# Kernel optimization log

Hardware: AMD Instinct MI355X
Metric: run time of the kernel (lower is better)

## Reference

```python
import jax, jax.numpy as jnp
import numpy as np
import math

H = 16          # n_head
N_EMBD = 1024
EPS = 1e-5      # torch LayerNorm default


def setup_inputs() -> dict:
    key = jax.random.key(0)
    ks = jax.random.split(key, 6)
    B, T, C = 2, 2048, 1024
    x = jax.random.normal(ks[0], (B, T, C), dtype=jnp.float32)
    s = 0.02  # GPT-2 style init scale keeps softmax logits sane
    Wq = jax.random.normal(ks[1], (C, N_EMBD), dtype=jnp.float32) * s
    Wk = jax.random.normal(ks[2], (C, N_EMBD), dtype=jnp.float32) * s
    Wv = jax.random.normal(ks[3], (C, N_EMBD), dtype=jnp.float32) * s
    Wo = jax.random.normal(ks[4], (N_EMBD, C), dtype=jnp.float32) * s
    return {
        "x": x,
        "Wq": Wq, "bq": jnp.zeros((N_EMBD,), jnp.float32),
        "Wk": Wk, "bk": jnp.zeros((N_EMBD,), jnp.float32),
        "Wv": Wv, "bv": jnp.zeros((N_EMBD,), jnp.float32),
        "Wo": Wo, "bo": jnp.zeros((C,), jnp.float32),
        "gamma": jnp.ones((C,), jnp.float32),
        "beta": jnp.zeros((C,), jnp.float32),
    }


def reference(x, Wq, bq, Wk, bk, Wv, bv, Wo, bo, gamma, beta):
    B, T, _ = x.shape
    Dh = N_EMBD // H
    # projections -> (B, H, T, Dh)
    def split_heads(y):
        return y.reshape(B, T, H, Dh).transpose(0, 2, 1, 3)
    q = split_heads(x @ Wq + bq)
    k = split_heads(x @ Wk + bk)
    v = split_heads(x @ Wv + bv)
    # naive causal attention: explicit (B,H,T,T) scores
    att = jnp.einsum("bhtd,bhsd->bhts", q, k) * (1.0 / math.sqrt(Dh))
    causal = jnp.tril(jnp.ones((T, T), dtype=bool))
    att = jnp.where(causal[None, None], att, -jnp.inf)
    att = jax.nn.softmax(att, axis=-1)
    o = jnp.einsum("bhts,bhsd->bhtd", att, v)
    o = o.transpose(0, 2, 1, 3).reshape(B, T, N_EMBD)
    y = o @ Wo + bo
    # LayerNorm (dropout is identity at p=0 / eval)
    mu = jnp.mean(y, axis=-1, keepdims=True)
    var = jnp.var(y, axis=-1, keepdims=True)
    return (y - mu) * jax.lax.rsqrt(var + EPS) * gamma + beta
```

## Files before the change

### kernel.cpp

```cpp
#include <hip/hip_runtime.h>
#include <stdint.h>
#include <stddef.h>

typedef __attribute__((ext_vector_type(8))) short short8;
typedef __attribute__((ext_vector_type(4))) float f32x4;
typedef __attribute__((ext_vector_type(16))) float f32x16;
typedef __attribute__((ext_vector_type(4))) unsigned short us4;
typedef __attribute__((ext_vector_type(4))) unsigned u32x4;

#define DEVI static __device__ __forceinline__

DEVI unsigned short f2bf(float f) {
  unsigned u = __builtin_bit_cast(unsigned, f);
  u += 0x7FFFu + ((u >> 16) & 1u);
  return (unsigned short)(u >> 16);
}

DEVI float bf2f(unsigned short u) {
  return __builtin_bit_cast(float, ((unsigned)u) << 16);
}

DEVI f32x4 mfma16(short8 a, short8 b, f32x4 c) {
  return __builtin_amdgcn_mfma_f32_16x16x32_bf16(a, b, c, 0, 0, 0);
}

DEVI f32x16 mfma32(short8 a, short8 b, f32x16 c) {
  return __builtin_amdgcn_mfma_f32_32x32x16_bf16(a, b, c, 0, 0, 0);
}

DEVI unsigned cvtpk(float lo, float hi) {
  unsigned r;
  asm("v_cvt_pk_bf16_f32 %0, %1, %2" : "=v"(r) : "v"(lo), "v"(hi));
  return r;
}

DEVI void plswap(unsigned& a, unsigned& b) {
  asm("v_permlane32_swap_b32 %0, %1" : "+v"(a), "+v"(b));
}

DEVI float ex2(float x) {
  float r;
  asm("v_exp_f32 %0, %1" : "=v"(r) : "v"(x));
  return r;
}

DEVI float mx3(float a, float b, float c) {
  float r;
  asm("v_max3_f32 %0, %1, %2, %3" : "=v"(r) : "v"(a), "v"(b), "v"(c));
  return r;
}

DEVI f32x16 zero16() {
  f32x16 z;
#pragma unroll
  for (int i = 0; i < 16; ++i) z[i] = 0.f;
  return z;
}

DEVI void glds16(const void* g, void* l) {
  __builtin_amdgcn_global_load_lds(
      (const __attribute__((address_space(1))) void*)g,
      (__attribute__((address_space(3))) void*)l, 16, 0, 0);
}

__global__ __launch_bounds__(256) void k_cvt_x(const float* __restrict__ x,
                                               unsigned short* __restrict__ xb) {
  size_t i = ((size_t)blockIdx.x * 256 + threadIdx.x) * 8;
  f32x4 a = *(const f32x4*)(x + i);
  f32x4 b = *(const f32x4*)(x + i + 4);
  short8 v;
#pragma unroll
  for (int j = 0; j < 4; ++j) {
    v[j] = (short)f2bf(a[j]);
    v[4 + j] = (short)f2bf(b[j]);
  }
  *(short8*)(xb + i) = v;
}

__global__ __launch_bounds__(256) void k_twT4(const float* __restrict__ W0,
                                              const float* __restrict__ W1,
                                              const float* __restrict__ W2,
                                              const float* __restrict__ W3,
                                              unsigned short* __restrict__ WT) {
  __shared__ float tile[64][65];
  const int z = blockIdx.z;
  const float* W = (z == 0) ? W0 : (z == 1) ? W1 : (z == 2) ? W2 : W3;
  unsigned short* out = WT + (size_t)z * 1024 * 1024;
  const int n0 = blockIdx.x * 64, k0 = blockIdx.y * 64;
  const int t = threadIdx.x, rr = t >> 4, cc = (t & 15) * 4;
#pragma unroll
  for (int i = 0; i < 4; ++i) {
    int row = i * 16 + rr;
    f32x4 v = *(const f32x4*)(W + (size_t)(k0 + row) * 1024 + n0 + cc);
#pragma unroll
    for (int j = 0; j < 4; ++j) tile[row][cc + j] = v[j];
  }
  __syncthreads();
#pragma unroll
  for (int i = 0; i < 4; ++i) {
    int nrow = i * 16 + rr;
    us4 u;
#pragma unroll
    for (int j = 0; j < 4; ++j) u[j] = f2bf(tile[cc + j][nrow]);
    *(us4*)(out + (size_t)(n0 + nrow) * 1024 + k0 + cc) = u;
  }
}

template <bool SWAP>
DEVI void gemm_core2(const unsigned short* __restrict__ A,
                     const unsigned short* __restrict__ Bt,
                     int mt, int nt, char* lds, f32x4 (&acc)[4][4]) {
  const int t = threadIdx.x;
  const int l = t & 63, c = l & 15, g = l >> 4;
  const int w = t >> 6, wr = w >> 1, wc = w & 1;
  const int srow = t >> 3;
  const int sxor = (((t & 7) ^ (srow & 7))) * 8;
  const unsigned short* Ab = A + (size_t)(mt * 128 + srow) * 1024 + sxor;
  const unsigned short* Bb = Bt + (size_t)(nt * 128 + srow) * 1024 + sxor;
  const int key = (c & 7);

  auto STAGE = [&](int kt, int buf) {
    char* lb = lds + buf * 32768;
#pragma unroll
    for (int i = 0; i < 4; ++i) {
      glds16(Ab + (size_t)i * 32 * 1024 + kt * 64, lb + i * 4096 + t * 16);
      glds16(Bb + (size_t)i * 32 * 1024 + kt * 64, lb + 16384 + i * 4096 + t * 16);
    }
  };

  STAGE(0, 0);
  asm volatile("s_waitcnt vmcnt(0)" ::: "memory");
  __builtin_amdgcn_s_barrier();
  asm volatile("" ::: "memory");
  for (int kt = 0; kt < 16; ++kt) {
    const int cur = kt & 1;
    if (kt < 15) STAGE(kt + 1, cur ^ 1);
    const char* lb = lds + cur * 32768;
#pragma unroll
    for (int ks = 0; ks < 2; ++ks) {
      short8 af[4], bfr[4];
#pragma unroll
      for (int m = 0; m < 4; ++m)
        af[m] = *(const short8*)(lb + (wr * 64 + m * 16 + c) * 128 +
                                 ((ks * 4 + g) ^ key) * 16);
#pragma unroll
      for (int n = 0; n < 4; ++n)
        bfr[n] = *(const short8*)(lb + 16384 + (wc * 64 + n * 16 + c) * 128 +
                                  ((ks * 4 + g) ^ key) * 16);
#pragma unroll
      for (int m = 0; m < 4; ++m)
#pragma unroll
        for (int n = 0; n < 4; ++n)
          acc[m][n] = SWAP ? mfma16(bfr[n], af[m], acc[m][n])
                           : mfma16(af[m], bfr[n], acc[m][n]);
    }
    asm volatile("s_waitcnt vmcnt(0)" ::: "memory");
    __builtin_amdgcn_s_barrier();
    asm volatile("" ::: "memory");
  }
}

__global__ __launch_bounds__(256) void k_gemm_qkv(
    const unsigned short* __restrict__ A,
    const unsigned short* __restrict__ Wf,
    const float* __restrict__ b0, const float* __restrict__ b1, const float* __restrict__ b2,
    unsigned short* __restrict__ O0, unsigned short* __restrict__ O1,
    unsigned short* __restrict__ O2) {
  __shared__ char lds[65536];
  const int mt = blockIdx.x, ntz = blockIdx.y;
  const int z = ntz >> 3, ntl = ntz & 7;
  const float* bias = (z == 0) ? b0 : (z == 1) ? b1 : b2;
  unsigned short* out = (z == 0) ? O0 : (z == 1) ? O1 : O2;
  f32x4 acc[4][4];
#pragma unroll
  for (int m = 0; m < 4; ++m)
#pragma unroll
    for (int n = 0; n < 4; ++n) acc[m][n] = (f32x4){0.f, 0.f, 0.f, 0.f};
  const int t = threadIdx.x, l = t & 63, c = l & 15, g = l >> 4;
  const int w = t >> 6, wr = w >> 1, wc = w & 1;
  if (z < 2) {
    gemm_core2<true>(A, Wf, mt, ntz, lds, acc);
    const float sc = (z == 0) ? 0.18033688011f : 1.0f;
#pragma unroll
    for (int n = 0; n < 4; ++n) {
      int colb = ntl * 128 + wc * 64 + n * 16 + 4 * g;
      f32x4 bv4 = *(const f32x4*)(bias + colb);
      int h = colb >> 6, d = colb & 63;
#pragma unroll
      for (int m = 0; m < 4; ++m) {
        int rowg = mt * 128 + wr * 64 + m * 16 + c;
        int b = rowg >> 11, tt = rowg & 2047;
        us4 u;
#pragma unroll
        for (int r = 0; r < 4; ++r) u[r] = f2bf((acc[m][n][r] + bv4[r]) * sc);
        *(us4*)(out + ((size_t)(b * 16 + h) * 2048 + tt) * 64 + d) = u;
      }
    }
  } else {
    gemm_core2<false>(A, Wf, mt, ntz, lds, acc);
#pragma unroll
    for (int n = 0; n < 4; ++n) {
      int colg = ntl * 128 + wc * 64 + n * 16 + c;
      float bvv = bias[colg];
      int h = colg >> 6, d = colg & 63;
#pragma unroll
      for (int m = 0; m < 4; ++m) {
        int rowg = mt * 128 + wr * 64 + m * 16 + 4 * g;
        int b = rowg >> 11, tt = rowg & 2047;
        us4 u;
#pragma unroll
        for (int r = 0; r < 4; ++r) u[r] = f2bf(acc[m][n][r] + bvv);
        *(us4*)(out + ((size_t)(b * 16 + h) * 64 + d) * 2048 + tt) = u;
      }
    }
  }
}

__global__ __launch_bounds__(256) void k_gemm_proj(const unsigned short* __restrict__ A,
                                                   const unsigned short* __restrict__ Bt,
                                                   const float* __restrict__ bias,
                                                   float* __restrict__ Y) {
  __shared__ char lds[65536];
  f32x4 acc[4][4];
#pragma unroll
  for (int m = 0; m < 4; ++m)
#pragma unroll
    for (int n = 0; n < 4; ++n) acc[m][n] = (f32x4){0.f, 0.f, 0.f, 0.f};
  const int mt = blockIdx.x, nt = blockIdx.y;
  gemm_core2<true>(A, Bt, mt, nt, lds, acc);
  const int t = threadIdx.x, l = t & 63, c = l & 15, g = l >> 4;
  const int w = t >> 6, wr = w >> 1, wc = w & 1;
#pragma unroll
  for (int n = 0; n < 4; ++n) {
    int colb = nt * 128 + wc * 64 + n * 16 + 4 * g;
    f32x4 bv4 = *(const f32x4*)(bias + colb);
#pragma unroll
    for (int m = 0; m < 4; ++m) {
      int rowg = mt * 128 + wr * 64 + m * 16 + c;
      f32x4 o;
#pragma unroll
      for (int r = 0; r < 4; ++r) o[r] = acc[m][n][r] + bv4[r];
      *(f32x4*)(Y + (size_t)rowg * 1024 + colb) = o;
    }
  }
}

__global__ __launch_bounds__(128) void k_attn5(const unsigned short* __restrict__ Q,
                                               const unsigned short* __restrict__ K,
                                               const unsigned short* __restrict__ VT,
                                               unsigned short* __restrict__ O,
                                               unsigned short* __restrict__ P,
                                               float* __restrict__ ML) {
  __shared__ char lds[32768];
  const int bid = blockIdx.x;
  int qt, c0, nt, mode, bh;
  if (bid < 512) {
    mode = 1; qt = 16 + (bid >> 5); c0 = 0; nt = 16; bh = bid & 31;
  } else {
    int rem = bid - 512;
    int v = 16 - (rem >> 6);
    int sub = rem & 63;
    bh = sub & 31;
    if (sub < 32) { mode = 0; qt = v - 1;  c0 = 0;  nt = v; }
    else          { mode = 2; qt = v + 15; c0 = 16; nt = v; }
  }
  const int t = threadIdx.x;
  const int w = t >> 6, l = t & 63;
  const int lq = l & 31, hi = l >> 5;
  const int q0 = qt * 64 + w * 32;
  const size_t kbase = (size_t)bh * 2048 * 64;
  const size_t vbase = (size_t)bh * 64 * 2048;
  const int srow = t >> 3;
  const int sx = ((t & 7) ^ (srow & 7)) * 8;

  short8 qf[4];
#pragma unroll
  for (int ds = 0; ds < 4; ++ds)
    qf[ds] = *(const short8*)(Q + kbase + (size_t)(q0 + lq) * 64 + 16 * ds + 8 * hi);

  auto STAGE = [&](int ktg, int buf) {
    const unsigned short* Kt = K + kbase + (size_t)ktg * 4096;
    const unsigned short* Vt = VT + vbase + ktg * 64;
    char* lb = lds + buf * 16384;
#pragma unroll
    for (int i = 0; i < 4; ++i) {
      int row = i * 16 + srow;
      glds16(Kt + (size_t)row * 64 + sx, lb + i * 2048 + t * 16);
      glds16(Vt + (size_t)row * 2048 + sx, lb + 8192 + i * 2048 + t * 16);
    }
  };

  f32x16 oacc[2];
  oacc[0] = zero16();
  oacc[1] = zero16();
  float m_s = -1e30f, l_s = 0.f;
  const int rx = lq & 7;

  STAGE(c0, 0);
  for (int kt = 0; kt < nt; ++kt) {
    asm volatile("s_waitcnt vmcnt(0)" ::: "memory");
    __builtin_amdgcn_s_barrier();
    asm volatile("" ::: "memory");
    if (kt + 1 < nt) STAGE(c0 + kt + 1, (kt + 1) & 1);
    const char* lb = lds + (kt & 1) * 16384;
    const int kv0 = (c0 + kt) * 64;
    short8 kf0[4], kf1[4];
#pragma unroll
    for (int ds = 0; ds < 4; ++ds) {
      int blk = ((ds * 2 + hi) ^ rx) * 16;
      kf0[ds] = *(const short8*)(lb + lq * 128 + blk);
      kf1[ds] = *(const short8*)(lb + (lq + 32) * 128 + blk);
    }
    f32x16 st0 = zero16(), st1 = zero16();
    __builtin_amdgcn_s_setprio(1);
#pragma unroll
    for (int ds = 0; ds < 4; ++ds) {
      st0 = mfma32(kf0[ds], qf[ds], st0);
      st1 = mfma32(kf1[ds], qf[ds], st1);
    }
    __builtin_amdgcn_s_setprio(0);
    short8 vf[2][4];
#pragma unroll
    for (int fd = 0; fd < 2; ++fd) {
      int d = fd * 32 + lq;
#pragma unroll
      for (int s = 0; s < 4; ++s)
        vf[fd][s] = *(const short8*)(lb + 8192 + d * 128 + (((s * 2 + hi) ^ rx) * 16));
    }
    if (mode != 1 && kt == nt - 1) {
      const int qg = q0 + lq;
#pragma unroll
      for (int r = 0; r < 16; ++r) {
        int kr = kv0 + (r & 3) + 8 * (r >> 2) + 4 * hi;
        if (kr > qg) st0[r] = -1e30f;
        if (kr + 32 > qg) st1[r] = -1e30f;
      }
    }
    float a8[8];
#pragma unroll
    for (int r = 0; r < 8; ++r)
      a8[r] = fmaxf(mx3(st0[r], st0[r + 8], st1[r]), st1[r + 8]);
    float mxv = mx3(mx3(a8[0], a8[1], a8[2]), mx3(a8[3], a8[4], a8[5]),
                    fmaxf(a8[6], a8[7]));
    mxv = fmaxf(mxv, __shfl_xor(mxv, 32, 64));
    if (!__all(mxv - m_s <= 11.5413f)) {
      float mnew = fmaxf(m_s, mxv);
      float corr = ex2(m_s - mnew);
      m_s = mnew;
      l_s *= corr;
#pragma unroll
      for (int r = 0; r < 16; ++r) {
        oacc[0][r] *= corr;
        oacc[1][r] *= corr;
      }
    }
    unsigned Wp[2][4][2];
    float gs[8];
#pragma unroll
    for (int f = 0; f < 2; ++f)
#pragma unroll
      for (int m4 = 0; m4 < 4; ++m4) {
        float p0 = ex2((f ? st1 : st0)[4 * m4 + 0] - m_s);
        float p1 = ex2((f ? st1 : st0)[4 * m4 + 1] - m_s);
        float p2 = ex2((f ? st1 : st0)[4 * m4 + 2] - m_s);
        float p3 = ex2((f ? st1 : st0)[4 * m4 + 3] - m_s);
        gs[f * 4 + m4] = (p0 + p1) + (p2 + p3);
        Wp[f][m4][0] = cvtpk(p0, p1);
        Wp[f][m4][1] = cvtpk(p2, p3);
      }
    float ps = ((gs[0] + gs[1]) + (gs[2] + gs[3])) + ((gs[4] + gs[5]) + (gs[6] + gs[7]));
    ps += __shfl_xor(ps, 32, 64);
    l_s += ps;
    __builtin_amdgcn_s_setprio(1);
#pragma unroll
    for (int s = 0; s < 4; ++s) {
      const int f = s >> 1, s2 = s & 1;
      unsigned a0 = Wp[f][2 * s2][0], b0 = Wp[f][2 * s2 + 1][0];
      unsigned a1 = Wp[f][2 * s2][1], b1 = Wp[f][2 * s2 + 1][1];
      plswap(a0, b0);
      plswap(a1, b1);
      u32x4 pw = {a0, a1, b0, b1};
      short8 pf = __builtin_bit_cast(short8, pw);
      oacc[0] = mfma32(vf[0][s], pf, oacc[0]);
      oacc[1] = mfma32(vf[1][s], pf, oacc[1]);
    }
    __builtin_amdgcn_s_setprio(0);
  }
  if (mode == 0) {
    const float inv = 1.0f / l_s;
    const int b = bh >> 4, h = bh & 15;
    unsigned short* orow = O + ((size_t)b * 2048 + q0 + lq) * 1024 + h * 64 + 4 * hi;
#pragma unroll
    for (int f = 0; f < 2; ++f)
#pragma unroll
      for (int m4 = 0; m4 < 4; ++m4) {
        us4 u;
#pragma unroll
        for (int rr = 0; rr < 4; ++rr) u[rr] = f2bf(oacc[f][4 * m4 + rr] * inv);
        *(us4*)(orow + f * 32 + m4 * 8) = u;
      }
  } else {
    const int pid = ((qt - 16) * 32 + bh) * 2 + (mode - 1);
    unsigned short* prow = P + (size_t)pid * 4096 + (w * 32 + lq) * 64 + 4 * hi;
#pragma unroll
    for (int f = 0; f < 2; ++f)
#pragma unroll
      for (int m4 = 0; m4 < 4; ++m4) {
        us4 u;
#pragma unroll
        for (int rr = 0; rr < 4; ++rr) u[rr] = f2bf(oacc[f][4 * m4 + rr]);
        *(us4*)(prow + f * 32 + m4 * 8) = u;
      }
    if (hi == 0) {
      ML[pid * 128 + w * 32 + lq] = m_s;
      ML[pid * 128 + 64 + w * 32 + lq] = l_s;
    }
  }
}

__global__ __launch_bounds__(64) void k_merge(const unsigned short* __restrict__ P,
                                              const float* __restrict__ ML,
                                              unsigned short* __restrict__ O) {
  const int blk = blockIdx.x;
  const int qt = 16 + (blk >> 5), bh = blk & 31;
  const int pidA = ((qt - 16) * 32 + bh) * 2, pidB = pidA + 1;
  const int r = threadIdx.x;
  float mA = ML[pidA * 128 + r], lA = ML[pidA * 128 + 64 + r];
  float mB = ML[pidB * 128 + r], lB = ML[pidB * 128 + 64 + r];
  float mM = fmaxf(mA, mB);
  float wA = ex2(mA - mM), wB = ex2(mB - mM);
  float inv = 1.f / (lA * wA + lB * wB);
  wA *= inv;
  wB *= inv;
  const unsigned short* pa = P + (size_t)pidA * 4096 + r * 64;
  const unsigned short* pb = P + (size_t)pidB * 4096 + r * 64;
  const int b = bh >> 4, h = bh & 15, q = qt * 64 + r;
  unsigned short* orow = O + ((size_t)b * 2048 + q) * 1024 + h * 64;
#pragma unroll
  for (int j = 0; j < 8; ++j) {
    short8 a = *(const short8*)(pa + j * 8);
    short8 c = *(const short8*)(pb + j * 8);
    short8 o;
#pragma unroll
    for (int k = 0; k < 8; ++k)
      o[k] = (short)f2bf(bf2f((unsigned short)a[k]) * wA +
                         bf2f((unsigned short)c[k]) * wB);
    *(short8*)(orow + j * 8) = o;
  }
}

__global__ __launch_bounds__(256) void k_ln(const float* __restrict__ Y,
                                            const float* __restrict__ gamma,
                                            const float* __restrict__ beta,
                                            float* __restrict__ out) {
  __shared__ float red[8];
  const int row = blockIdx.x, t = threadIdx.x, w = t >> 6, l = t & 63;
  const float* yr = Y + (size_t)row * 1024;
  f32x4 v = *(const f32x4*)(yr + t * 4);
  float s = v[0] + v[1] + v[2] + v[3];
  float ss = v[0] * v[0] + v[1] * v[1] + v[2] * v[2] + v[3] * v[3];
#pragma unroll
  for (int d = 1; d < 64; d <<= 1) {
    s += __shfl_xor(s, d, 64);
    ss += __shfl_xor(ss, d, 64);
  }
  if (l == 0) {
    red[w] = s;
    red[4 + w] = ss;
  }
  __syncthreads();
  s = red[0] + red[1] + red[2] + red[3];
  ss = red[4] + red[5] + red[6] + red[7];
  float mean = s * (1.f / 1024.f);
  float var = ss * (1.f / 1024.f) - mean * mean;
  float rstd = rsqrtf(var + 1e-5f);
  f32x4 gv = *(const f32x4*)(gamma + t * 4);
  f32x4 bv = *(const f32x4*)(beta + t * 4);
  f32x4 ov;
#pragma unroll
  for (int j = 0; j < 4; ++j) ov[j] = (v[j] - mean) * rstd * gv[j] + bv[j];
  *(f32x4*)(out + (size_t)row * 1024 + t * 4) = ov;
}

extern "C" void kernel_launch(void* const* d_in, const int* in_sizes, int n_in,
                              void* d_out, int out_size, void* d_ws, size_t ws_size,
                              hipStream_t stream) {
  (void)in_sizes; (void)n_in; (void)out_size; (void)ws_size;
  const float* x = (const float*)d_in[0];
  const float* Wq = (const float*)d_in[1];
  const float* bq = (const float*)d_in[2];
  const float* Wk = (const float*)d_in[3];
  const float* bk = (const float*)d_in[4];
  const float* Wv = (const float*)d_in[5];
  const float* bv = (const float*)d_in[6];
  const float* Wo = (const float*)d_in[7];
  const float* bo = (const float*)d_in[8];
  const float* gamma = (const float*)d_in[9];
  const float* beta = (const float*)d_in[10];
  char* ws = (char*)d_ws;
  const size_t MB = 1024 * 1024;
  unsigned short* xb = (unsigned short*)(ws);
  unsigned short* WT = (unsigned short*)(ws + 8 * MB);
  unsigned short* WoT = (unsigned short*)(ws + 14 * MB);
  unsigned short* Qb = (unsigned short*)(ws + 16 * MB);
  unsigned short* Kb = (unsigned short*)(ws + 24 * MB);
  unsigned short* VTb = (unsigned short*)(ws + 32 * MB);
  unsigned short* Ob = (unsigned short*)(ws + 40 * MB);
  float* Y = (float*)(ws + 16 * MB);
  unsigned short* Pp = (unsigned short*)(ws);
  float* MLp = (float*)(ws + 8 * MB);

  k_cvt_x<<<2048, 256, 0, stream>>>(x, xb);
  k_twT4<<<dim3(16, 16, 4), 256, 0, stream>>>(Wq, Wk, Wv, Wo, WT);
  k_gemm_qkv<<<dim3(32, 24), 256, 0, stream>>>(xb, WT, bq, bk, bv, Qb, Kb, VTb);
  k_attn5<<<1536, 128, 0, stream>>>(Qb, Kb, VTb, Ob, Pp, MLp);
  k_merge<<<512, 64, 0, stream>>>(Pp, MLp, Ob);
  k_gemm_proj<<<dim3(32, 8), 256, 0, stream>>>(Ob, WoT, bo, Y);
  k_ln<<<4096, 256, 0, stream>>>(Y, gamma, beta, (float*)d_out);
}
```

Measured before the change: 118.6 us.

## Halve attention KV tile to 32 and skip fully masked tiles per wave

The attention kernel now steps through keys in 32-row tiles instead of 64, so its LDS footprint halves and the V tile uses a new swizzled layout. Each wave gets its own trip count, letting the lower-query wave skip the last fully masked tile on diagonal blocks instead of computing and discarding it. The cost is twice as many loop iterations, each with a barrier and a smaller MFMA batch. The smaller LDS use may allow more blocks to be resident per CU.

```diff
diff --git a/kernel.cpp b/kernel.cpp
--- a/kernel.cpp
+++ b/kernel.cpp
@@ -245,24 +245,24 @@
   }
 }
 
-__global__ __launch_bounds__(128) void k_attn5(const unsigned short* __restrict__ Q,
+__global__ __launch_bounds__(128) void k_attn6(const unsigned short* __restrict__ Q,
                                                const unsigned short* __restrict__ K,
                                                const unsigned short* __restrict__ VT,
                                                unsigned short* __restrict__ O,
                                                unsigned short* __restrict__ P,
                                                float* __restrict__ ML) {
-  __shared__ char lds[32768];
+  __shared__ char lds[16384];
   const int bid = blockIdx.x;
-  int qt, c0, nt, mode, bh;
+  int qt, c0, NT, mode, bh;
   if (bid < 512) {
-    mode = 1; qt = 16 + (bid >> 5); c0 = 0; nt = 16; bh = bid & 31;
+    mode = 1; qt = 16 + (bid >> 5); c0 = 0; NT = 32; bh = bid & 31;
   } else {
     int rem = bid - 512;
     int v = 16 - (rem >> 6);
     int sub = rem & 63;
     bh = sub & 31;
-    if (sub < 32) { mode = 0; qt = v - 1;  c0 = 0;  nt = v; }
-    else          { mode = 2; qt = v + 15; c0 = 16; nt = v; }
+    if (sub < 32) { mode = 0; qt = v - 1;  c0 = 0;  NT = 2 * v; }
+    else          { mode = 2; qt = v + 15; c0 = 32; NT = 2 * v; }
   }
   const int t = threadIdx.x;
   const int w = t >> 6, l = t & 63;
@@ -270,8 +270,8 @@
   const int q0 = qt * 64 + w * 32;
   const size_t kbase = (size_t)bh * 2048 * 64;
   const size_t vbase = (size_t)bh * 64 * 2048;
-  const int srow = t >> 3;
-  const int sx = ((t & 7) ^ (srow & 7)) * 8;
+  const int srow = t >> 3, sblk = t & 7;
+  const int my_nt = (mode == 1) ? 32 : (NT - 1 + w);
 
   short8 qf[4];
 #pragma unroll
@@ -279,14 +279,17 @@
     qf[ds] = *(const short8*)(Q + kbase + (size_t)(q0 + lq) * 64 + 16 * ds + 8 * hi);
 
   auto STAGE = [&](int ktg, int buf) {
-    const unsigned short* Kt = K + kbase + (size_t)ktg * 4096;
-    const unsigned short* Vt = VT + vbase + ktg * 64;
-    char* lb = lds + buf * 16384;
-#pragma unroll
-    for (int i = 0; i < 4; ++i) {
+    const unsigned short* Kt = K + kbase + (size_t)ktg * 32 * 64;
+    char* lb = lds + buf * 8192;
+#pragma unroll
+    for (int i = 0; i < 2; ++i) {
       int row = i * 16 + srow;
-      glds16(Kt + (size_t)row * 64 + sx, lb + i * 2048 + t * 16);
-      glds16(Vt + (size_t)row * 2048 + sx, lb + 8192 + i * 2048 + t * 16);
+      glds16(Kt + (size_t)row * 64 + (size_t)((sblk ^ (row & 7)) * 8),
+             lb + i * 2048 + t * 16);
+      int bp = sblk ^ (row & 7);
+      int d = row * 2 + (bp >> 2);
+      glds16(VT + vbase + (size_t)d * 2048 + (size_t)(ktg * 32 + (bp & 3) * 8),
+             lb + 4096 + i * 2048 + t * 16);
     }
   };
 
@@ -297,94 +300,86 @@
   const int rx = lq & 7;
 
   STAGE(c0, 0);
-  for (int kt = 0; kt < nt; ++kt) {
+  for (int kt = 0; kt < NT; ++kt) {
     asm volatile("s_waitcnt vmcnt(0)" ::: "memory");
     __builtin_amdgcn_s_barrier();
     asm volatile("" ::: "memory");
-    if (kt + 1 < nt) STAGE(c0 + kt + 1, (kt + 1) & 1);
-    const char* lb = lds + (kt & 1) * 16384;
-    const int kv0 = (c0 + kt) * 64;
-    short8 kf0[4], kf1[4];
-#pragma unroll
-    for (int ds = 0; ds < 4; ++ds) {
-      int blk = ((ds * 2 + hi) ^ rx) * 16;
-      kf0[ds] = *(const short8*)(lb + lq * 128 + blk);
-      kf1[ds] = *(const short8*)(lb + (lq + 32) * 128 + blk);
-    }
-    f32x16 st0 = zero16(), st1 = zero16();
-    __builtin_amdgcn_s_setprio(1);
-#pragma unroll
-    for (int ds = 0; ds < 4; ++ds) {
-      st0 = mfma32(kf0[ds], qf[ds], st0);
-      st1 = mfma32(kf1[ds], qf[ds], st1);
-    }
-    __builtin_amdgcn_s_setprio(0);
-    short8 vf[2][4];
-#pragma unroll
-    for (int fd = 0; fd < 2; ++fd) {
-      int d = fd * 32 + lq;
-#pragma unroll
-      for (int s = 0; s < 4; ++s)
-        vf[fd][s] = *(const short8*)(lb + 8192 + d * 128 + (((s * 2 + hi) ^ rx) * 16));
-    }
-    if (mode != 1 && kt == nt - 1) {
-      const int qg = q0 + lq;
-#pragma unroll
-      for (int r = 0; r < 16; ++r) {
-        int kr = kv0 + (r & 3) + 8 * (r >> 2) + 4 * hi;
-        if (kr > qg) st0[r] = -1e30f;
-        if (kr + 32 > qg) st1[r] = -1e30f;
-      }
-    }
-    float a8[8];
-#pragma unroll
-    for (int r = 0; r < 8; ++r)
-      a8[r] = fmaxf(mx3(st0[r], st0[r + 8], st1[r]), st1[r + 8]);
-    float mxv = mx3(mx3(a8[0], a8[1], a8[2]), mx3(a8[3], a8[4], a8[5]),
-                    fmaxf(a8[6], a8[7]));
-    mxv = fmaxf(mxv, __shfl_xor(mxv, 32, 64));
-    if (!__all(mxv - m_s <= 11.5413f)) {
-      float mnew = fmaxf(m_s, mxv);
-      float corr = ex2(m_s - mnew);
-      m_s = mnew;
-      l_s *= corr;
-#pragma unroll
-      for (int r = 0; r < 16; ++r) {
-        oacc[0][r] *= corr;
-        oacc[1][r] *= corr;
-      }
-    }
-    unsigned Wp[2][4][2];
-    float gs[8];
-#pragma unroll
-    for (int f = 0; f < 2; ++f)
+    if (kt + 1 < NT) STAGE(c0 + kt + 1, (kt + 1) & 1);
+    if (kt < my_nt) {
+      const char* lb = lds + (kt & 1) * 8192;
+      const int kv0 = (c0 + kt) * 32;
+      short8 kf[4];
+#pragma unroll
+      for (int ds = 0; ds < 4; ++ds)
+        kf[ds] = *(const short8*)(lb + lq * 128 + (((ds * 2 + hi) ^ rx) * 16));
+      f32x16 st = zero16();
+      __builtin_amdgcn_s_setprio(1);
+#pragma unroll
+      for (int ds = 0; ds < 4; ++ds) st = mfma32(kf[ds], qf[ds], st);
+      __builtin_amdgcn_s_setprio(0);
+      short8 vf[2][2];
+#pragma unroll
+      for (int fd = 0; fd < 2; ++fd) {
+        int d2 = fd * 16 + (lq >> 1);
+        int vkey = d2 & 7;
+#pragma unroll
+        for (int s = 0; s < 2; ++s)
+          vf[fd][s] = *(const short8*)(lb + 4096 + d2 * 128 +
+                                       ((((lq & 1) * 4 + s * 2 + hi) ^ vkey) * 16));
+      }
+      if (mode != 1 && kt == my_nt - 1) {
+        const int qg = q0 + lq;
+#pragma unroll
+        for (int r = 0; r < 16; ++r) {
+          int kr = kv0 + (r & 3) + 8 * (r >> 2) + 4 * hi;
+          if (kr > qg) st[r] = -1e30f;
+        }
+      }
+      float a0 = mx3(st[0], st[1], st[2]), a1 = mx3(st[3], st[4], st[5]);
+      float a2 = mx3(st[6], st[7], st[8]), a3 = mx3(st[9], st[10], st[11]);
+      float a4 = mx3(st[12], st[13], st[14]);
+      float mxv = fmaxf(mx3(a0, a1, a2), mx3(a3, a4, st[15]));
+      mxv = fmaxf(mxv, __shfl_xor(mxv, 32, 64));
+      if (!__all(mxv - m_s <= 11.5413f)) {
+        float mnew = fmaxf(m_s, mxv);
+        float corr = ex2(m_s - mnew);
+        m_s = mnew;
+        l_s *= corr;
+#pragma unroll
+        for (int r = 0; r < 16; ++r) {
+          oacc[0][r] *= corr;
+          oacc[1][r] *= corr;
+        }
+      }
+      unsigned Wp[4][2];
+      float gs[4];
 #pragma unroll
       for (int m4 = 0; m4 < 4; ++m4) {
-        float p0 = ex2((f ? st1 : st0)[4 * m4 + 0] - m_s);
-        float p1 = ex2((f ? st1 : st0)[4 * m4 + 1] - m_s);
-        float p2 = ex2((f ? st1 : st0)[4 * m4 + 2] - m_s);
-        float p3 = ex2((f ? st1 : st0)[4 * m4 + 3] - m_s);
-        gs[f * 4 + m4] = (p0 + p1) + (p2 + p3);
-        Wp[f][m4][0] = cvtpk(p0, p1);
-        Wp[f][m4][1] = cvtpk(p2, p3);
-      }
-    float ps = ((gs[0] + gs[1]) + (gs[2] + gs[3])) + ((gs[4] + gs[5]) + (gs[6] + gs[7]));
-    ps += __shfl_xor(ps, 32, 64);
-    l_s += ps;
-    __builtin_amdgcn_s_setprio(1);
-#pragma unroll
-    for (int s = 0; s < 4; ++s) {
-      const int f = s >> 1, s2 = s & 1;
-      unsigned a0 = Wp[f][2 * s2][0], b0 = Wp[f][2 * s2 + 1][0];
-      unsigned a1 = Wp[f][2 * s2][1], b1 = Wp[f][2 * s2 + 1][1];
-      plswap(a0, b0);
-      plswap(a1, b1);
-      u32x4 pw = {a0, a1, b0, b1};
-      short8 pf = __builtin_bit_cast(short8, pw);
-      oacc[0] = mfma32(vf[0][s], pf, oacc[0]);
-      oacc[1] = mfma32(vf[1][s], pf, oacc[1]);
-    }
-    __builtin_amdgcn_s_setprio(0);
+        float p0 = ex2(st[4 * m4 + 0] - m_s);
+        float p1 = ex2(st[4 * m4 + 1] - m_s);
+        float p2 = ex2(st[4 * m4 + 2] - m_s);
+        float p3 = ex2(st[4 * m4 + 3] - m_s);
+        gs[m4] = (p0 + p1) + (p2 + p3);
+        Wp[m4][0] = cvtpk(p0, p1);
+        Wp[m4][1] = cvtpk(p2, p3);
+      }
+      float ps = (gs[0] + gs[1]) + (gs[2] + gs[3]);
+      ps += __shfl_xor(ps, 32, 64);
+      l_s += ps;
+      __builtin_amdgcn_s_setprio(1);
+#pragma unroll
+      for (int s = 0; s < 2; ++s) {
+        unsigned x0 = Wp[2 * s][0], y0 = Wp[2 * s + 1][0];
+        unsigned x1 = Wp[2 * s][1], y1 = Wp[2 * s + 1][1];
+        plswap(x0, y0);
+        plswap(x1, y1);
+        u32x4 pw = {x0, x1, y0, y1};
+        short8 pf = __builtin_bit_cast(short8, pw);
+        oacc[0] = mfma32(vf[0][s], pf, oacc[0]);
+        oacc[1] = mfma32(vf[1][s], pf, oacc[1]);
+      }
+      __builtin_amdgcn_s_setprio(0);
+    }
   }
   if (mode == 0) {
     const float inv = 1.0f / l_s;
@@ -513,7 +508,7 @@
   k_cvt_x<<<2048, 256, 0, stream>>>(x, xb);
   k_twT4<<<dim3(16, 16, 4), 256, 0, stream>>>(Wq, Wk, Wv, Wo, WT);
   k_gemm_qkv<<<dim3(32, 24), 256, 0, stream>>>(xb, WT, bq, bk, bv, Qb, Kb, VTb);
-  k_attn5<<<1536, 128, 0, stream>>>(Qb, Kb, VTb, Ob, Pp, MLp);
+  k_attn6<<<1536, 128, 0, stream>>>(Qb, Kb, VTb, Ob, Pp, MLp);
   k_merge<<<512, 64, 0, stream>>>(Pp, MLp, Ob);
   k_gemm_proj<<<dim3(32, 8), 256, 0, stream>>>(Ob, WoT, bo, Y);
   k_ln<<<4096, 256, 0, stream>>>(Y, gamma, beta, (float*)d_out);
```

After: 126.9 us. 7.0% more time.
